# Kernel tuning notes

Hardware: AMD Instinct MI355X
Metric: run time of the kernel (lower is better)

Reference implementation:

```python
import jax, jax.numpy as jnp
import numpy as np

DIM = 512
HEADS = 8
DIM_HEAD = 64
DIM_INNER = HEADS * DIM_HEAD  # 512
EPS = 1e-12


def setup_inputs() -> dict:
    key = jax.random.key(0)
    ks = jax.random.split(key, 5)
    B, X, Y, N = 8, 32, 32, 1024
    fmap = jax.random.normal(ks[0], (B, DIM, X, Y), dtype=jnp.float32)
    context = jax.random.normal(ks[1], (B, N, DIM), dtype=jnp.float32)
    gamma_fmap = jnp.ones((DIM, 1, 1), dtype=jnp.float32)
    gamma_ctx = jnp.ones((DIM,), dtype=jnp.float32)
    Wq = jax.random.normal(ks[2], (DIM_INNER, DIM), dtype=jnp.float32) * 0.02
    Wkv = jax.random.normal(ks[3], (2 * DIM_INNER, DIM), dtype=jnp.float32) * 0.02
    Wout = jax.random.normal(ks[4], (DIM, DIM_INNER), dtype=jnp.float32) * 0.02
    return {"fmap": fmap, "context": context, "gamma_fmap": gamma_fmap,
            "gamma_ctx": gamma_ctx, "Wq": Wq, "Wkv": Wkv, "Wout": Wout}


def _channel_rmsnorm(x, gamma):
    # F.normalize(x, dim=1) * sqrt(dim) * gamma ; x: [b, c, x, y]
    norm = jnp.sqrt(jnp.sum(x * x, axis=1, keepdims=True))
    normed = x / jnp.maximum(norm, EPS)
    return normed * (DIM ** 0.5) * gamma


def _rmsnorm(x, gamma):
    # F.normalize(x, dim=-1) * sqrt(dim) * gamma ; x: [b, n, d]
    norm = jnp.sqrt(jnp.sum(x * x, axis=-1, keepdims=True))
    normed = x / jnp.maximum(norm, EPS)
    return normed * (DIM ** 0.5) * gamma


def reference(fmap, context, gamma_fmap, gamma_ctx, Wq, Wkv, Wout):
    B, _, X, Y = fmap.shape
    N = context.shape[1]
    H, D = HEADS, DIM_HEAD
    scale = D ** -0.5

    fm = _channel_rmsnorm(fmap, gamma_fmap)          # [b, c, x, y]
    ctx = _rmsnorm(context, gamma_ctx)               # [b, n, c]

    # 1x1 conv == channel matmul
    q = jnp.einsum('bcxy,ec->bexy', fm, Wq)          # [b, h*d, x, y]
    kv = jnp.einsum('bnc,ec->bne', ctx, Wkv)         # [b, n, 2*h*d]
    k, v = jnp.split(kv, 2, axis=-1)

    # q: b (h d) x y -> (b h) (x y) d
    q = q.reshape(B, H, D, X * Y).transpose(0, 1, 3, 2).reshape(B * H, X * Y, D)
    # k, v: b n (h d) -> (b h) n d
    k = k.reshape(B, N, H, D).transpose(0, 2, 1, 3).reshape(B * H, N, D)
    v = v.reshape(B, N, H, D).transpose(0, 2, 1, 3).reshape(B * H, N, D)

    # Euclidean cdist: sqrt(||q||^2 + ||k||^2 - 2 q.k)
    q2 = jnp.sum(q * q, axis=-1)                     # [bh, i]
    k2 = jnp.sum(k * k, axis=-1)                     # [bh, j]
    qk = jnp.einsum('bid,bjd->bij', q, k)            # [bh, i, j]
    dist = jnp.sqrt(jnp.maximum(q2[:, :, None] + k2[:, None, :] - 2.0 * qk, 0.0))
    sim = -dist * scale
    attn = jax.nn.softmax(sim, axis=-1)

    out = jnp.einsum('bij,bjd->bid', attn, v)        # [bh, xy, d]
    # (b h) (x y) d -> b (h d) x y
    out = out.reshape(B, H, X * Y, D).transpose(0, 1, 3, 2).reshape(B, H * D, X, Y)
    return jnp.einsum('bexy,de->bdxy', out, Wout)    # [b, dim, x, y]
```

## Files before the change

kernel.cpp:

```cpp
#include <hip/hip_runtime.h>
#include <hip/hip_bf16.h>
#include <math.h>

#define BATCH 8
#define CDIM 512
#define XY 1024
#define NCTX 1024
#define HEADS 8
#define DHEAD 64
#define EINNER 512
#define E2 1024

#define SQRT_DIM 22.627416997969522f
#define NEG_SL2E -0.18033688011112042f

typedef short bf16x8 __attribute__((ext_vector_type(8)));
typedef float f32x4 __attribute__((ext_vector_type(4)));
typedef unsigned short u16;
typedef u16 ushort8v __attribute__((ext_vector_type(8)));
typedef u16 ushort4v __attribute__((ext_vector_type(4)));

__device__ __forceinline__ u16 f2bf(float x) {
    return __builtin_bit_cast(u16, __float2bfloat16(x));
}
__device__ __forceinline__ float bf2f(u16 h) {
    unsigned int u = ((unsigned int)h) << 16;
    return __builtin_bit_cast(float, u);
}

__global__ __launch_bounds__(256) void k_fmap_prep(const float* __restrict__ fmap,
                                                   u16* __restrict__ fmTh,
                                                   u16* __restrict__ fmTl,
                                                   float* __restrict__ fscale) {
    const int blk = blockIdx.x, b = blk >> 5, x0 = (blk & 31) * 32;
    const int xy = threadIdx.x & 31, cg = threadIdx.x >> 5;
    const float* p = fmap + (size_t)b * CDIM * XY + x0 + xy;
    u16* ph = fmTh + ((size_t)b * 1024 + x0 + xy) * 512 + cg * 64;
    u16* pl = fmTl + ((size_t)b * 1024 + x0 + xy) * 512 + cg * 64;
    float ss = 0.f;
#pragma unroll
    for (int ii = 0; ii < 8; ++ii) {
        ushort8v h8, l8;
#pragma unroll
        for (int j = 0; j < 8; ++j) {
            float v = p[(size_t)(cg * 64 + ii * 8 + j) * XY];
            ss = fmaf(v, v, ss);
            u16 hh = f2bf(v);
            h8[j] = hh;
            l8[j] = f2bf(v - bf2f(hh));
        }
        *(ushort8v*)(ph + ii * 8) = h8;
        *(ushort8v*)(pl + ii * 8) = l8;
    }
    __shared__ float red[8][33];
    red[cg][xy] = ss;
    __syncthreads();
    if (threadIdx.x < 32) {
        float s = red[0][xy] + red[1][xy] + red[2][xy] + red[3][xy]
                + red[4][xy] + red[5][xy] + red[6][xy] + red[7][xy];
        fscale[b * XY + x0 + xy] = SQRT_DIM / fmaxf(sqrtf(s), 1e-12f);
    }
}

__global__ __launch_bounds__(256) void k_ctx_scale(const float* __restrict__ ctx,
                                                   float* __restrict__ cscale) {
    int row = blockIdx.x * 4 + (threadIdx.x >> 6);
    int lane = threadIdx.x & 63;
    const float* p = ctx + (size_t)row * CDIM;
    float ss = 0.f;
#pragma unroll
    for (int k = 0; k < CDIM / 64; ++k) {
        float v = p[lane + 64 * k];
        ss = fmaf(v, v, ss);
    }
#pragma unroll
    for (int off = 32; off; off >>= 1) ss += __shfl_down(ss, off, 64);
    if (lane == 0) cscale[row] = SQRT_DIM / fmaxf(sqrtf(ss), 1e-12f);
}

__global__ __launch_bounds__(256) void k_wsplit(const float* __restrict__ src,
                                                const float* __restrict__ gamma,
                                                u16* __restrict__ dh,
                                                u16* __restrict__ dl, int n8) {
    int i = blockIdx.x * 256 + threadIdx.x;
    if (i >= n8) return;
    size_t base = (size_t)i * 8;
    int k0 = (int)(base & 511);
    float4 a = *(const float4*)(src + base);
    float4 b4 = *(const float4*)(src + base + 4);
    float v[8] = {a.x, a.y, a.z, a.w, b4.x, b4.y, b4.z, b4.w};
    if (gamma) {
        float4 g0 = *(const float4*)(gamma + k0);
        float4 g1 = *(const float4*)(gamma + k0 + 4);
        v[0] *= g0.x; v[1] *= g0.y; v[2] *= g0.z; v[3] *= g0.w;
        v[4] *= g1.x; v[5] *= g1.y; v[6] *= g1.z; v[7] *= g1.w;
    }
    ushort8v h8, l8;
#pragma unroll
    for (int j = 0; j < 8; ++j) {
        u16 hh = f2bf(v[j]);
        h8[j] = hh;
        l8[j] = f2bf(v[j] - bf2f(hh));
    }
    *(ushort8v*)(dh + base) = h8;
    *(ushort8v*)(dl + base) = l8;
}

__global__ __launch_bounds__(256, 4) void k_gemm_q(
    const u16* __restrict__ fmTh, const u16* __restrict__ fmTl,
    const u16* __restrict__ wqh, const u16* __restrict__ wql,
    const float* __restrict__ fscale,
    u16* __restrict__ qh_, u16* __restrict__ ql_, float* __restrict__ q2g) {
    const int b = blockIdx.z, h = blockIdx.y, xy0 = blockIdx.x * 64;
    const int t = threadIdx.x, w = t >> 6, lane = t & 63;
    const int c = lane & 15, g = lane >> 4;
    const u16* Ah = fmTh + ((size_t)b * 1024 + xy0 + 16 * w + c) * 512 + 8 * g;
    const u16* Al = fmTl + ((size_t)b * 1024 + xy0 + 16 * w + c) * 512 + 8 * g;
    const u16* Bh0 = wqh + ((size_t)(h * 64) + c) * 512 + 8 * g;
    const u16* Bl0 = wql + ((size_t)(h * 64) + c) * 512 + 8 * g;
    f32x4 acc[4] = {{0.f,0.f,0.f,0.f},{0.f,0.f,0.f,0.f},{0.f,0.f,0.f,0.f},{0.f,0.f,0.f,0.f}};
#pragma unroll 2
    for (int k0 = 0; k0 < 512; k0 += 32) {
        bf16x8 ah = *(const bf16x8*)(Ah + k0);
        bf16x8 al = *(const bf16x8*)(Al + k0);
#pragma unroll
        for (int ct = 0; ct < 4; ++ct) {
            bf16x8 bh_ = *(const bf16x8*)(Bh0 + (size_t)ct * 16 * 512 + k0);
            bf16x8 bl_ = *(const bf16x8*)(Bl0 + (size_t)ct * 16 * 512 + k0);
            acc[ct] = __builtin_amdgcn_mfma_f32_16x16x32_bf16(ah, bh_, acc[ct], 0, 0, 0);
            acc[ct] = __builtin_amdgcn_mfma_f32_16x16x32_bf16(ah, bl_, acc[ct], 0, 0, 0);
            acc[ct] = __builtin_amdgcn_mfma_f32_16x16x32_bf16(al, bh_, acc[ct], 0, 0, 0);
        }
    }
    const int bh = b * 8 + h;
    const float4 fs4 = *(const float4*)(fscale + b * 1024 + xy0 + 16 * w + 4 * g);
    const float fsr[4] = {fs4.x, fs4.y, fs4.z, fs4.w};
    float s2[4] = {0.f, 0.f, 0.f, 0.f};
#pragma unroll
    for (int ct = 0; ct < 4; ++ct)
#pragma unroll
        for (int r = 0; r < 4; ++r) {
            float v = acc[ct][r] * fsr[r];
            u16 hh = f2bf(v);
            size_t adr = ((size_t)bh * 1024 + xy0 + 16 * w + 4 * g + r) * 64 + 16 * ct + c;
            qh_[adr] = hh;
            ql_[adr] = f2bf(v - bf2f(hh));
            s2[r] = fmaf(v, v, s2[r]);
        }
#pragma unroll
    for (int r = 0; r < 4; ++r) {
        float s = s2[r];
        s += __shfl_xor(s, 1, 64);
        s += __shfl_xor(s, 2, 64);
        s += __shfl_xor(s, 4, 64);
        s += __shfl_xor(s, 8, 64);
        if (c == 0) q2g[(size_t)bh * 1024 + xy0 + 16 * w + 4 * g + r] = s;
    }
}

__global__ __launch_bounds__(256, 4) void k_gemm_kv(
    const float* __restrict__ ctx, const u16* __restrict__ wkvh,
    const u16* __restrict__ wkvl, const float* __restrict__ cscale,
    u16* __restrict__ khi, u16* __restrict__ klo,
    u16* __restrict__ vthi, u16* __restrict__ vtlo, float* __restrict__ k2g) {
    const int b = blockIdx.z, et = blockIdx.y, n0 = blockIdx.x * 64;
    const int t = threadIdx.x, w = t >> 6, lane = t & 63;
    const int c = lane & 15, g = lane >> 4;
    __shared__ u16 vl[4][2][64][24];
    const float* Ap = ctx + ((size_t)b * 1024 + n0 + 16 * w + c) * 512 + 8 * g;
    const u16* Bh0 = wkvh + ((size_t)(et * 64) + c) * 512 + 8 * g;
    const u16* Bl0 = wkvl + ((size_t)(et * 64) + c) * 512 + 8 * g;
    f32x4 acc[4] = {{0.f,0.f,0.f,0.f},{0.f,0.f,0.f,0.f},{0.f,0.f,0.f,0.f},{0.f,0.f,0.f,0.f}};
#pragma unroll 2
    for (int k0 = 0; k0 < 512; k0 += 32) {
        float4 a0 = *(const float4*)(Ap + k0);
        float4 a1 = *(const float4*)(Ap + k0 + 4);
        float av[8] = {a0.x, a0.y, a0.z, a0.w, a1.x, a1.y, a1.z, a1.w};
        bf16x8 ah, al;
#pragma unroll
        for (int j = 0; j < 8; ++j) {
            u16 hh = f2bf(av[j]);
            ah[j] = (short)hh;
            al[j] = (short)f2bf(av[j] - bf2f(hh));
        }
#pragma unroll
        for (int ct = 0; ct < 4; ++ct) {
            bf16x8 bh_ = *(const bf16x8*)(Bh0 + (size_t)ct * 16 * 512 + k0);
            bf16x8 bl_ = *(const bf16x8*)(Bl0 + (size_t)ct * 16 * 512 + k0);
            acc[ct] = __builtin_amdgcn_mfma_f32_16x16x32_bf16(ah, bh_, acc[ct], 0, 0, 0);
            acc[ct] = __builtin_amdgcn_mfma_f32_16x16x32_bf16(ah, bl_, acc[ct], 0, 0, 0);
            acc[ct] = __builtin_amdgcn_mfma_f32_16x16x32_bf16(al, bh_, acc[ct], 0, 0, 0);
        }
    }
    const float4 cs4 = *(const float4*)(cscale + b * 1024 + n0 + 16 * w + 4 * g);
    const float csr[4] = {cs4.x, cs4.y, cs4.z, cs4.w};
    if (et < 8) {
        const int bh = b * 8 + et;
        float s2[4] = {0.f, 0.f, 0.f, 0.f};
#pragma unroll
        for (int ct = 0; ct < 4; ++ct)
#pragma unroll
            for (int r = 0; r < 4; ++r) {
                float v = acc[ct][r] * csr[r];
                u16 hh = f2bf(v);
                size_t adr = ((size_t)bh * 1024 + n0 + 16 * w + 4 * g + r) * 64 + 16 * ct + c;
                khi[adr] = hh;
                klo[adr] = f2bf(v - bf2f(hh));
                s2[r] = fmaf(v, v, s2[r]);
            }
#pragma unroll
        for (int r = 0; r < 4; ++r) {
            float s = s2[r];
            s += __shfl_xor(s, 1, 64);
            s += __shfl_xor(s, 2, 64);
            s += __shfl_xor(s, 4, 64);
            s += __shfl_xor(s, 8, 64);
            if (c == 0) k2g[(size_t)bh * 1024 + n0 + 16 * w + 4 * g + r] = s;
        }
    } else {
        const int h = et - 8, bh = b * 8 + h;
#pragma unroll
        for (int ct = 0; ct < 4; ++ct)
#pragma unroll
            for (int r = 0; r < 4; ++r) {
                float v = acc[ct][r] * csr[r];
                u16 hh = f2bf(v);
                vl[w][0][16 * ct + c][4 * g + r] = hh;
                vl[w][1][16 * ct + c][4 * g + r] = f2bf(v - bf2f(hh));
            }
        const int d = lane;
        ushort8v h0 = *(const ushort8v*)(&vl[w][0][d][0]);
        ushort8v h1 = *(const ushort8v*)(&vl[w][0][d][8]);
        ushort8v l0 = *(const ushort8v*)(&vl[w][1][d][0]);
        ushort8v l1 = *(const ushort8v*)(&vl[w][1][d][8]);
        size_t base = ((size_t)bh * 64 + d) * 1024 + n0 + 16 * w;
        *(ushort8v*)(vthi + base) = h0;
        *(ushort8v*)(vthi + base + 8) = h1;
        *(ushort8v*)(vtlo + base) = l0;
        *(ushort8v*)(vtlo + base + 8) = l1;
    }
}

__global__ __launch_bounds__(256, 4) void k_gemm_out(
    const u16* __restrict__ wouth, const u16* __restrict__ woutl,
    const u16* __restrict__ aoTh, const u16* __restrict__ aoTl,
    float* __restrict__ out) {
    const int b = blockIdx.z, m0 = blockIdx.y * 64, n0 = blockIdx.x * 64;
    const int t = threadIdx.x, w = t >> 6, lane = t & 63;
    const int c = lane & 15, g = lane >> 4;
    const u16* Ah = wouth + ((size_t)(m0 + 16 * w) + c) * 512 + 8 * g;
    const u16* Al = woutl + ((size_t)(m0 + 16 * w) + c) * 512 + 8 * g;
    const u16* Bh0 = aoTh + ((size_t)b * 1024 + n0 + c) * 512 + 8 * g;
    const u16* Bl0 = aoTl + ((size_t)b * 1024 + n0 + c) * 512 + 8 * g;
    f32x4 acc[4] = {{0.f,0.f,0.f,0.f},{0.f,0.f,0.f,0.f},{0.f,0.f,0.f,0.f},{0.f,0.f,0.f,0.f}};
#pragma unroll 2
    for (int k0 = 0; k0 < 512; k0 += 32) {
        bf16x8 ah = *(const bf16x8*)(Ah + k0);
        bf16x8 al = *(const bf16x8*)(Al + k0);
#pragma unroll
        for (int ct = 0; ct < 4; ++ct) {
            bf16x8 bh_ = *(const bf16x8*)(Bh0 + (size_t)ct * 16 * 512 + k0);
            bf16x8 bl_ = *(const bf16x8*)(Bl0 + (size_t)ct * 16 * 512 + k0);
            acc[ct] = __builtin_amdgcn_mfma_f32_16x16x32_bf16(ah, bh_, acc[ct], 0, 0, 0);
            acc[ct] = __builtin_amdgcn_mfma_f32_16x16x32_bf16(ah, bl_, acc[ct], 0, 0, 0);
            acc[ct] = __builtin_amdgcn_mfma_f32_16x16x32_bf16(al, bh_, acc[ct], 0, 0, 0);
        }
    }
#pragma unroll
    for (int ct = 0; ct < 4; ++ct)
#pragma unroll
        for (int r = 0; r < 4; ++r)
            out[((size_t)b * 512 + m0 + 16 * w + 4 * g + r) * 1024 + n0 + 16 * ct + c] =
                acc[ct][r];
}

__global__ __launch_bounds__(256, 4) void k_attn_mfma(
    const u16* __restrict__ q_h, const u16* __restrict__ q_l,
    const u16* __restrict__ khi, const u16* __restrict__ klo,
    const u16* __restrict__ vthi, const u16* __restrict__ vtlo,
    const float* __restrict__ q2g, const float* __restrict__ k2g,
    u16* __restrict__ aoTh, u16* __restrict__ aoTl) {
    const int bh = blockIdx.x;
    const int i0 = blockIdx.y * 32;
    const int t = threadIdx.x;
    const int w = t >> 6;
    const int rg = w >> 1;
    const int jh = w & 1;
    const int lane = t & 63;
    const int c = lane & 15, g = lane >> 4;

    __shared__ __align__(16) char pool[4 * 4864];
    u16* psth = (u16*)(pool + w * 4864);
    u16* pstl = psth + 16 * 76;
    __shared__ float msh[4][16];
    __shared__ float lsh[4][16];

    const int qrow = i0 + 16 * rg + c;
    const u16* qhp = q_h + ((size_t)bh * 1024 + qrow) * 64 + 8 * g;
    const u16* qlp = q_l + ((size_t)bh * 1024 + qrow) * 64 + 8 * g;
    bf16x8 qh[2], ql[2];
    qh[0] = *(const bf16x8*)(qhp);
    qh[1] = *(const bf16x8*)(qhp + 32);
    ql[0] = *(const bf16x8*)(qlp);
    ql[1] = *(const bf16x8*)(qlp + 32);
    const float q2c = q2g[(size_t)bh * 1024 + qrow];

    const u16* khb = khi + (size_t)bh * NCTX * 64;
    const u16* klb = klo + (size_t)bh * NCTX * 64;
    const u16* vhb = vthi + (size_t)bh * 64 * NCTX;
    const u16* vlb = vtlo + (size_t)bh * 64 * NCTX;
    const float* k2b = k2g + (size_t)bh * NCTX;

    f32x4 acc_o[4] = {{0.f,0.f,0.f,0.f},{0.f,0.f,0.f,0.f},{0.f,0.f,0.f,0.f},{0.f,0.f,0.f,0.f}};
    float m_run = -1e30f, l_run = 0.f;

    const int jbeg = jh * 512, jend = jbeg + 512;
    for (int j0 = jbeg; j0 < jend; j0 += 64) {
        float s[4][4];
#pragma unroll
        for (int mm = 0; mm < 4; ++mm) {
            const u16* kr_h = khb + (size_t)(j0 + 16 * mm + c) * 64 + 8 * g;
            const u16* kr_l = klb + (size_t)(j0 + 16 * mm + c) * 64 + 8 * g;
            f32x4 acc = {0.f, 0.f, 0.f, 0.f};
#pragma unroll
            for (int kk = 0; kk < 2; ++kk) {
                bf16x8 kh_ = *(const bf16x8*)(kr_h + 32 * kk);
                bf16x8 kl_ = *(const bf16x8*)(kr_l + 32 * kk);
                acc = __builtin_amdgcn_mfma_f32_16x16x32_bf16(kh_, qh[kk], acc, 0, 0, 0);
                acc = __builtin_amdgcn_mfma_f32_16x16x32_bf16(kh_, ql[kk], acc, 0, 0, 0);
                acc = __builtin_amdgcn_mfma_f32_16x16x32_bf16(kl_, qh[kk], acc, 0, 0, 0);
            }
            const float4 kv4 = *(const float4*)(k2b + j0 + 16 * mm + 4 * g);
            const float k2a[4] = {kv4.x, kv4.y, kv4.z, kv4.w};
#pragma unroll
            for (int r = 0; r < 4; ++r) {
                float d2 = fmaf(-2.f, acc[r], q2c + k2a[r]);
                s[mm][r] = NEG_SL2E * sqrtf(fmaxf(d2, 0.f));
            }
        }
        float mt = s[0][0];
#pragma unroll
        for (int mm = 0; mm < 4; ++mm)
#pragma unroll
            for (int r = 0; r < 4; ++r) mt = fmaxf(mt, s[mm][r]);
        mt = fmaxf(mt, __shfl_xor(mt, 16, 64));
        mt = fmaxf(mt, __shfl_xor(mt, 32, 64));
        float mn = fmaxf(m_run, mt);
        float alpha = exp2f(m_run - mn);
        m_run = mn;
        float sum = 0.f;
#pragma unroll
        for (int mm = 0; mm < 4; ++mm)
#pragma unroll
            for (int r = 0; r < 4; ++r) {
                float e = exp2f(s[mm][r] - mn);
                s[mm][r] = e;
                sum += e;
            }
        sum += __shfl_xor(sum, 16, 64);
        sum += __shfl_xor(sum, 32, 64);
        l_run = l_run * alpha + sum;
#pragma unroll
        for (int dt = 0; dt < 4; ++dt)
#pragma unroll
            for (int r = 0; r < 4; ++r) acc_o[dt][r] *= alpha;

#pragma unroll
        for (int mm = 0; mm < 4; ++mm) {
            ushort4v h4, l4;
#pragma unroll
            for (int r = 0; r < 4; ++r) {
                u16 hh = f2bf(s[mm][r]);
                h4[r] = hh;
                l4[r] = f2bf(s[mm][r] - bf2f(hh));
            }
            *(ushort4v*)(psth + c * 76 + 16 * mm + 4 * g) = h4;
            *(ushort4v*)(pstl + c * 76 + 16 * mm + 4 * g) = l4;
        }
        bf16x8 ph[2], pl[2];
#pragma unroll
        for (int kk = 0; kk < 2; ++kk) {
            ph[kk] = *(const bf16x8*)(psth + c * 76 + 32 * kk + 8 * g);
            pl[kk] = *(const bf16x8*)(pstl + c * 76 + 32 * kk + 8 * g);
        }
#pragma unroll
        for (int dt = 0; dt < 4; ++dt) {
            const u16* vr_h = vhb + (size_t)(16 * dt + c) * NCTX + j0 + 8 * g;
            const u16* vr_l = vlb + (size_t)(16 * dt + c) * NCTX + j0 + 8 * g;
#pragma unroll
            for (int kk = 0; kk < 2; ++kk) {
                bf16x8 vh_ = *(const bf16x8*)(vr_h + 32 * kk);
                bf16x8 vl_ = *(const bf16x8*)(vr_l + 32 * kk);
                acc_o[dt] = __builtin_amdgcn_mfma_f32_16x16x32_bf16(vh_, ph[kk], acc_o[dt], 0, 0, 0);
                acc_o[dt] = __builtin_amdgcn_mfma_f32_16x16x32_bf16(vh_, pl[kk], acc_o[dt], 0, 0, 0);
                acc_o[dt] = __builtin_amdgcn_mfma_f32_16x16x32_bf16(vl_, ph[kk], acc_o[dt], 0, 0, 0);
            }
        }
    }

    float* pfw = (float*)(pool + w * 4864);
#pragma unroll
    for (int dt = 0; dt < 4; ++dt)
#pragma unroll
        for (int r = 0; r < 4; ++r)
            pfw[(16 * dt + 4 * g + r) * 18 + c] = acc_o[dt][r];
    if (g == 0) { msh[w][c] = m_run; lsh[w][c] = l_run; }
    __syncthreads();

    {
        const int cq = t & 15, rgq = (t >> 4) & 1, dblk = t >> 5;
        const int wA = 2 * rgq, wB = wA + 1;
        const float m1 = msh[wA][cq], m2 = msh[wB][cq];
        const float l1 = lsh[wA][cq], l2 = lsh[wB][cq];
        const float M = fmaxf(m1, m2);
        const float e1 = exp2f(m1 - M), e2 = exp2f(m2 - M);
        const float inv = 1.f / (e1 * l1 + e2 * l2);
        const float w1 = e1 * inv, w2 = e2 * inv;
        const float* pA = (const float*)(pool + wA * 4864);
        const float* pB = (const float*)(pool + wB * 4864);
        const int b = bh >> 3, h = bh & 7;
        const int xy = i0 + 16 * rgq + cq;
        ushort8v h8, l8;
#pragma unroll
        for (int dd = 0; dd < 8; ++dd) {
            int d = dblk * 8 + dd;
            float o = w1 * pA[d * 18 + cq] + w2 * pB[d * 18 + cq];
            u16 hh = f2bf(o);
            h8[dd] = hh;
            l8[dd] = f2bf(o - bf2f(hh));
        }
        size_t adr = ((size_t)b * 1024 + xy) * 512 + h * 64 + dblk * 8;
        *(ushort8v*)(aoTh + adr) = h8;
        *(ushort8v*)(aoTl + adr) = l8;
    }
}

extern "C" void kernel_launch(void* const* d_in, const int* in_sizes, int n_in,
                              void* d_out, int out_size, void* d_ws, size_t ws_size,
                              hipStream_t stream) {
    const float* fmap    = (const float*)d_in[0];
    const float* context = (const float*)d_in[1];
    const float* gfm     = (const float*)d_in[2];
    const float* gctx    = (const float*)d_in[3];
    const float* Wq      = (const float*)d_in[4];
    const float* Wkv     = (const float*)d_in[5];
    const float* Wout    = (const float*)d_in[6];
    float* out = (float*)d_out;

    char* wsb = (char*)d_ws;
    u16* fmTh = (u16*)(wsb);
    u16* fmTl = (u16*)(wsb + (8u << 20));
    u16* khi  = fmTh;
    u16* klo  = fmTl;
    u16* vthi = (u16*)(wsb + (16u << 20));
    u16* vtlo = (u16*)(wsb + (24u << 20));
    u16* q_h  = (u16*)(wsb + (32u << 20));
    u16* q_l  = (u16*)(wsb + (40u << 20));
    u16* aoTh = (u16*)(wsb + (48u << 20));
    u16* aoTl = (u16*)(wsb + (56u << 20));
    u16* wouth = (u16*)(wsb);
    u16* woutl = (u16*)(wsb + 524288 * 2);

    u16* du = (u16*)d_out;
    u16* wkvh = du;
    u16* wkvl = du + 524288;
    u16* wqh  = du + 1048576;
    u16* wql  = du + 1310720;
    float* df = (float*)((char*)d_out + (4u << 20));
    float* q2g    = df;
    float* k2g    = df + 65536;
    float* fscale = df + 131072;
    float* cscale = df + 139264;

    k_fmap_prep<<<256, 256, 0, stream>>>(fmap, fmTh, fmTl, fscale);
    k_ctx_scale<<<2048, 256, 0, stream>>>(context, cscale);
    k_wsplit<<<128, 256, 0, stream>>>(Wq, gfm, wqh, wql, 512 * 512 / 8);
    k_wsplit<<<256, 256, 0, stream>>>(Wkv, gctx, wkvh, wkvl, 1024 * 512 / 8);

    k_gemm_q<<<dim3(16, 8, BATCH), 256, 0, stream>>>(
        fmTh, fmTl, wqh, wql, fscale, q_h, q_l, q2g);

    k_gemm_kv<<<dim3(16, 16, BATCH), 256, 0, stream>>>(
        context, wkvh, wkvl, cscale, khi, klo, vthi, vtlo, k2g);

    k_attn_mfma<<<dim3(64, 32), 256, 0, stream>>>(
        q_h, q_l, khi, klo, vthi, vtlo, q2g, k2g, aoTh, aoTl);

    k_wsplit<<<128, 256, 0, stream>>>(Wout, nullptr, wouth, woutl, 512 * 512 / 8);

    k_gemm_out<<<dim3(16, 8, BATCH), 256, 0, stream>>>(
        wouth, woutl, aoTh, aoTl, out);
}
```

Baseline: 653.9 us.

## Pad GEMM row strides, pre-split context to bf16, use fast sqrt/exp in attention

```diff
diff --git a/kernel.cpp b/kernel.cpp
--- a/kernel.cpp
+++ b/kernel.cpp
@@ -11,6 +11,9 @@
 #define EINNER 512
 #define E2 1024
 
+#define GSTR 640
+#define VSTR 1152
+
 #define SQRT_DIM 22.627416997969522f
 #define NEG_SL2E -0.18033688011112042f
 
@@ -26,6 +29,16 @@
 __device__ __forceinline__ float bf2f(u16 h) {
     unsigned int u = ((unsigned int)h) << 16;
     return __builtin_bit_cast(float, u);
+}
+__device__ __forceinline__ float fast_sqrt(float x) {
+    float r;
+    asm("v_sqrt_f32 %0, %1" : "=v"(r) : "v"(x));
+    return r;
+}
+__device__ __forceinline__ float fast_exp2(float x) {
+    float r;
+    asm("v_exp_f32 %0, %1" : "=v"(r) : "v"(x));
+    return r;
 }
 
 __global__ __launch_bounds__(256) void k_fmap_prep(const float* __restrict__ fmap,
@@ -35,8 +48,8 @@
     const int blk = blockIdx.x, b = blk >> 5, x0 = (blk & 31) * 32;
     const int xy = threadIdx.x & 31, cg = threadIdx.x >> 5;
     const float* p = fmap + (size_t)b * CDIM * XY + x0 + xy;
-    u16* ph = fmTh + ((size_t)b * 1024 + x0 + xy) * 512 + cg * 64;
-    u16* pl = fmTl + ((size_t)b * 1024 + x0 + xy) * 512 + cg * 64;
+    u16* ph = fmTh + ((size_t)b * 1024 + x0 + xy) * GSTR + cg * 64;
+    u16* pl = fmTl + ((size_t)b * 1024 + x0 + xy) * GSTR + cg * 64;
     float ss = 0.f;
 #pragma unroll
     for (int ii = 0; ii < 8; ++ii) {
@@ -62,17 +75,27 @@
     }
 }
 
-__global__ __launch_bounds__(256) void k_ctx_scale(const float* __restrict__ ctx,
-                                                   float* __restrict__ cscale) {
-    int row = blockIdx.x * 4 + (threadIdx.x >> 6);
-    int lane = threadIdx.x & 63;
-    const float* p = ctx + (size_t)row * CDIM;
+__global__ __launch_bounds__(256) void k_ctx_prep(const float* __restrict__ ctx,
+                                                  u16* __restrict__ ctxh,
+                                                  u16* __restrict__ ctxl,
+                                                  float* __restrict__ cscale) {
+    const int row = blockIdx.x * 4 + (threadIdx.x >> 6);
+    const int lane = threadIdx.x & 63;
+    const float* p = ctx + (size_t)row * CDIM + lane * 8;
+    float4 a0 = *(const float4*)(p);
+    float4 a1 = *(const float4*)(p + 4);
+    float v[8] = {a0.x, a0.y, a0.z, a0.w, a1.x, a1.y, a1.z, a1.w};
     float ss = 0.f;
-#pragma unroll
-    for (int k = 0; k < CDIM / 64; ++k) {
-        float v = p[lane + 64 * k];
-        ss = fmaf(v, v, ss);
-    }
+    ushort8v h8, l8;
+#pragma unroll
+    for (int j = 0; j < 8; ++j) {
+        ss = fmaf(v[j], v[j], ss);
+        u16 hh = f2bf(v[j]);
+        h8[j] = hh;
+        l8[j] = f2bf(v[j] - bf2f(hh));
+    }
+    *(ushort8v*)(ctxh + (size_t)row * GSTR + lane * 8) = h8;
+    *(ushort8v*)(ctxl + (size_t)row * GSTR + lane * 8) = l8;
 #pragma unroll
     for (int off = 32; off; off >>= 1) ss += __shfl_down(ss, off, 64);
     if (lane == 0) cscale[row] = SQRT_DIM / fmaxf(sqrtf(ss), 1e-12f);
@@ -86,6 +109,7 @@
     if (i >= n8) return;
     size_t base = (size_t)i * 8;
     int k0 = (int)(base & 511);
+    size_t row = base >> 9;
     float4 a = *(const float4*)(src + base);
     float4 b4 = *(const float4*)(src + base + 4);
     float v[8] = {a.x, a.y, a.z, a.w, b4.x, b4.y, b4.z, b4.w};
@@ -102,8 +126,9 @@
         h8[j] = hh;
         l8[j] = f2bf(v[j] - bf2f(hh));
     }
-    *(ushort8v*)(dh + base) = h8;
-    *(ushort8v*)(dl + base) = l8;
+    size_t dst = row * GSTR + k0;
+    *(ushort8v*)(dh + dst) = h8;
+    *(ushort8v*)(dl + dst) = l8;
 }
 
 __global__ __launch_bounds__(256, 4) void k_gemm_q(
@@ -114,10 +139,10 @@
     const int b = blockIdx.z, h = blockIdx.y, xy0 = blockIdx.x * 64;
     const int t = threadIdx.x, w = t >> 6, lane = t & 63;
     const int c = lane & 15, g = lane >> 4;
-    const u16* Ah = fmTh + ((size_t)b * 1024 + xy0 + 16 * w + c) * 512 + 8 * g;
-    const u16* Al = fmTl + ((size_t)b * 1024 + xy0 + 16 * w + c) * 512 + 8 * g;
-    const u16* Bh0 = wqh + ((size_t)(h * 64) + c) * 512 + 8 * g;
-    const u16* Bl0 = wql + ((size_t)(h * 64) + c) * 512 + 8 * g;
+    const u16* Ah = fmTh + ((size_t)b * 1024 + xy0 + 16 * w + c) * GSTR + 8 * g;
+    const u16* Al = fmTl + ((size_t)b * 1024 + xy0 + 16 * w + c) * GSTR + 8 * g;
+    const u16* Bh0 = wqh + ((size_t)(h * 64) + c) * GSTR + 8 * g;
+    const u16* Bl0 = wql + ((size_t)(h * 64) + c) * GSTR + 8 * g;
     f32x4 acc[4] = {{0.f,0.f,0.f,0.f},{0.f,0.f,0.f,0.f},{0.f,0.f,0.f,0.f},{0.f,0.f,0.f,0.f}};
 #pragma unroll 2
     for (int k0 = 0; k0 < 512; k0 += 32) {
@@ -125,8 +150,8 @@
         bf16x8 al = *(const bf16x8*)(Al + k0);
 #pragma unroll
         for (int ct = 0; ct < 4; ++ct) {
-            bf16x8 bh_ = *(const bf16x8*)(Bh0 + (size_t)ct * 16 * 512 + k0);
-            bf16x8 bl_ = *(const bf16x8*)(Bl0 + (size_t)ct * 16 * 512 + k0);
+            bf16x8 bh_ = *(const bf16x8*)(Bh0 + (size_t)ct * 16 * GSTR + k0);
+            bf16x8 bl_ = *(const bf16x8*)(Bl0 + (size_t)ct * 16 * GSTR + k0);
             acc[ct] = __builtin_amdgcn_mfma_f32_16x16x32_bf16(ah, bh_, acc[ct], 0, 0, 0);
             acc[ct] = __builtin_amdgcn_mfma_f32_16x16x32_bf16(ah, bl_, acc[ct], 0, 0, 0);
             acc[ct] = __builtin_amdgcn_mfma_f32_16x16x32_bf16(al, bh_, acc[ct], 0, 0, 0);
@@ -159,34 +184,28 @@
 }
 
 __global__ __launch_bounds__(256, 4) void k_gemm_kv(
-    const float* __restrict__ ctx, const u16* __restrict__ wkvh,
-    const u16* __restrict__ wkvl, const float* __restrict__ cscale,
+    const u16* __restrict__ ctxh, const u16* __restrict__ ctxl,
+    const u16* __restrict__ wkvh, const u16* __restrict__ wkvl,
+    const float* __restrict__ cscale,
     u16* __restrict__ khi, u16* __restrict__ klo,
     u16* __restrict__ vthi, u16* __restrict__ vtlo, float* __restrict__ k2g) {
     const int b = blockIdx.z, et = blockIdx.y, n0 = blockIdx.x * 64;
     const int t = threadIdx.x, w = t >> 6, lane = t & 63;
     const int c = lane & 15, g = lane >> 4;
     __shared__ u16 vl[4][2][64][24];
-    const float* Ap = ctx + ((size_t)b * 1024 + n0 + 16 * w + c) * 512 + 8 * g;
-    const u16* Bh0 = wkvh + ((size_t)(et * 64) + c) * 512 + 8 * g;
-    const u16* Bl0 = wkvl + ((size_t)(et * 64) + c) * 512 + 8 * g;
+    const u16* Ah = ctxh + ((size_t)b * 1024 + n0 + 16 * w + c) * GSTR + 8 * g;
+    const u16* Al = ctxl + ((size_t)b * 1024 + n0 + 16 * w + c) * GSTR + 8 * g;
+    const u16* Bh0 = wkvh + ((size_t)(et * 64) + c) * GSTR + 8 * g;
+    const u16* Bl0 = wkvl + ((size_t)(et * 64) + c) * GSTR + 8 * g;
     f32x4 acc[4] = {{0.f,0.f,0.f,0.f},{0.f,0.f,0.f,0.f},{0.f,0.f,0.f,0.f},{0.f,0.f,0.f,0.f}};
 #pragma unroll 2
     for (int k0 = 0; k0 < 512; k0 += 32) {
-        float4 a0 = *(const float4*)(Ap + k0);
-        float4 a1 = *(const float4*)(Ap + k0 + 4);
-        float av[8] = {a0.x, a0.y, a0.z, a0.w, a1.x, a1.y, a1.z, a1.w};
-        bf16x8 ah, al;
-#pragma unroll
-        for (int j = 0; j < 8; ++j) {
-            u16 hh = f2bf(av[j]);
-            ah[j] = (short)hh;
-            al[j] = (short)f2bf(av[j] - bf2f(hh));
-        }
+        bf16x8 ah = *(const bf16x8*)(Ah + k0);
+        bf16x8 al = *(const bf16x8*)(Al + k0);
 #pragma unroll
         for (int ct = 0; ct < 4; ++ct) {
-            bf16x8 bh_ = *(const bf16x8*)(Bh0 + (size_t)ct * 16 * 512 + k0);
-            bf16x8 bl_ = *(const bf16x8*)(Bl0 + (size_t)ct * 16 * 512 + k0);
+            bf16x8 bh_ = *(const bf16x8*)(Bh0 + (size_t)ct * 16 * GSTR + k0);
+            bf16x8 bl_ = *(const bf16x8*)(Bl0 + (size_t)ct * 16 * GSTR + k0);
             acc[ct] = __builtin_amdgcn_mfma_f32_16x16x32_bf16(ah, bh_, acc[ct], 0, 0, 0);
             acc[ct] = __builtin_amdgcn_mfma_f32_16x16x32_bf16(ah, bl_, acc[ct], 0, 0, 0);
             acc[ct] = __builtin_amdgcn_mfma_f32_16x16x32_bf16(al, bh_, acc[ct], 0, 0, 0);
@@ -233,7 +252,7 @@
         ushort8v h1 = *(const ushort8v*)(&vl[w][0][d][8]);
         ushort8v l0 = *(const ushort8v*)(&vl[w][1][d][0]);
         ushort8v l1 = *(const ushort8v*)(&vl[w][1][d][8]);
-        size_t base = ((size_t)bh * 64 + d) * 1024 + n0 + 16 * w;
+        size_t base = ((size_t)bh * 64 + d) * VSTR + n0 + 16 * w;
         *(ushort8v*)(vthi + base) = h0;
         *(ushort8v*)(vthi + base + 8) = h1;
         *(ushort8v*)(vtlo + base) = l0;
@@ -248,10 +267,10 @@
     const int b = blockIdx.z, m0 = blockIdx.y * 64, n0 = blockIdx.x * 64;
     const int t = threadIdx.x, w = t >> 6, lane = t & 63;
     const int c = lane & 15, g = lane >> 4;
-    const u16* Ah = wouth + ((size_t)(m0 + 16 * w) + c) * 512 + 8 * g;
-    const u16* Al = woutl + ((size_t)(m0 + 16 * w) + c) * 512 + 8 * g;
-    const u16* Bh0 = aoTh + ((size_t)b * 1024 + n0 + c) * 512 + 8 * g;
-    const u16* Bl0 = aoTl + ((size_t)b * 1024 + n0 + c) * 512 + 8 * g;
+    const u16* Ah = wouth + ((size_t)(m0 + 16 * w) + c) * GSTR + 8 * g;
+    const u16* Al = woutl + ((size_t)(m0 + 16 * w) + c) * GSTR + 8 * g;
+    const u16* Bh0 = aoTh + ((size_t)b * 1024 + n0 + c) * GSTR + 8 * g;
+    const u16* Bl0 = aoTl + ((size_t)b * 1024 + n0 + c) * GSTR + 8 * g;
     f32x4 acc[4] = {{0.f,0.f,0.f,0.f},{0.f,0.f,0.f,0.f},{0.f,0.f,0.f,0.f},{0.f,0.f,0.f,0.f}};
 #pragma unroll 2
     for (int k0 = 0; k0 < 512; k0 += 32) {
@@ -259,8 +278,8 @@
         bf16x8 al = *(const bf16x8*)(Al + k0);
 #pragma unroll
         for (int ct = 0; ct < 4; ++ct) {
-            bf16x8 bh_ = *(const bf16x8*)(Bh0 + (size_t)ct * 16 * 512 + k0);
-            bf16x8 bl_ = *(const bf16x8*)(Bl0 + (size_t)ct * 16 * 512 + k0);
+            bf16x8 bh_ = *(const bf16x8*)(Bh0 + (size_t)ct * 16 * GSTR + k0);
+            bf16x8 bl_ = *(const bf16x8*)(Bl0 + (size_t)ct * 16 * GSTR + k0);
             acc[ct] = __builtin_amdgcn_mfma_f32_16x16x32_bf16(ah, bh_, acc[ct], 0, 0, 0);
             acc[ct] = __builtin_amdgcn_mfma_f32_16x16x32_bf16(ah, bl_, acc[ct], 0, 0, 0);
             acc[ct] = __builtin_amdgcn_mfma_f32_16x16x32_bf16(al, bh_, acc[ct], 0, 0, 0);
@@ -305,22 +324,29 @@
     ql[1] = *(const bf16x8*)(qlp + 32);
     const float q2c = q2g[(size_t)bh * 1024 + qrow];
 
-    const u16* khb = khi + (size_t)bh * NCTX * 64;
-    const u16* klb = klo + (size_t)bh * NCTX * 64;
-    const u16* vhb = vthi + (size_t)bh * 64 * NCTX;
-    const u16* vlb = vtlo + (size_t)bh * 64 * NCTX;
-    const float* k2b = k2g + (size_t)bh * NCTX;
+    const int jbeg = jh * 512;
+    const u16* kh_p = khi + (size_t)bh * NCTX * 64 + (size_t)(jbeg + c) * 64 + 8 * g;
+    const u16* kl_p = klo + (size_t)bh * NCTX * 64 + (size_t)(jbeg + c) * 64 + 8 * g;
+    const u16* kh_p2 = kh_p + 2048;
+    const u16* kl_p2 = kl_p + 2048;
+    const float* k2p = k2g + (size_t)bh * NCTX + jbeg + 4 * g;
+    const u16* vh_p[4];
+    const u16* vl_p[4];
+#pragma unroll
+    for (int dt = 0; dt < 4; ++dt) {
+        vh_p[dt] = vthi + ((size_t)bh * 64 + 16 * dt + c) * VSTR + jbeg + 8 * g;
+        vl_p[dt] = vtlo + ((size_t)bh * 64 + 16 * dt + c) * VSTR + jbeg + 8 * g;
+    }
 
     f32x4 acc_o[4] = {{0.f,0.f,0.f,0.f},{0.f,0.f,0.f,0.f},{0.f,0.f,0.f,0.f},{0.f,0.f,0.f,0.f}};
     float m_run = -1e30f, l_run = 0.f;
 
-    const int jbeg = jh * 512, jend = jbeg + 512;
-    for (int j0 = jbeg; j0 < jend; j0 += 64) {
+    for (int it = 0; it < 8; ++it) {
         float s[4][4];
 #pragma unroll
         for (int mm = 0; mm < 4; ++mm) {
-            const u16* kr_h = khb + (size_t)(j0 + 16 * mm + c) * 64 + 8 * g;
-            const u16* kr_l = klb + (size_t)(j0 + 16 * mm + c) * 64 + 8 * g;
+            const u16* kr_h = (mm < 2 ? kh_p : kh_p2) + (mm & 1) * 1024;
+            const u16* kr_l = (mm < 2 ? kl_p : kl_p2) + (mm & 1) * 1024;
             f32x4 acc = {0.f, 0.f, 0.f, 0.f};
 #pragma unroll
             for (int kk = 0; kk < 2; ++kk) {
@@ -330,12 +356,12 @@
                 acc = __builtin_amdgcn_mfma_f32_16x16x32_bf16(kh_, ql[kk], acc, 0, 0, 0);
                 acc = __builtin_amdgcn_mfma_f32_16x16x32_bf16(kl_, qh[kk], acc, 0, 0, 0);
             }
-            const float4 kv4 = *(const float4*)(k2b + j0 + 16 * mm + 4 * g);
+            const float4 kv4 = *(const float4*)(k2p + 16 * mm);
             const float k2a[4] = {kv4.x, kv4.y, kv4.z, kv4.w};
 #pragma unroll
             for (int r = 0; r < 4; ++r) {
                 float d2 = fmaf(-2.f, acc[r], q2c + k2a[r]);
-                s[mm][r] = NEG_SL2E * sqrtf(fmaxf(d2, 0.f));
+                s[mm][r] = NEG_SL2E * fast_sqrt(fmaxf(d2, 0.f));
             }
         }
         float mt = s[0][0];
@@ -346,14 +372,14 @@
         mt = fmaxf(mt, __shfl_xor(mt, 16, 64));
         mt = fmaxf(mt, __shfl_xor(mt, 32, 64));
         float mn = fmaxf(m_run, mt);
-        float alpha = exp2f(m_run - mn);
+        float alpha = fast_exp2(m_run - mn);
         m_run = mn;
         float sum = 0.f;
 #pragma unroll
         for (int mm = 0; mm < 4; ++mm)
 #pragma unroll
             for (int r = 0; r < 4; ++r) {
-                float e = exp2f(s[mm][r] - mn);
+                float e = fast_exp2(s[mm][r] - mn);
                 s[mm][r] = e;
                 sum += e;
             }
@@ -385,17 +411,19 @@
         }
 #pragma unroll
         for (int dt = 0; dt < 4; ++dt) {
-            const u16* vr_h = vhb + (size_t)(16 * dt + c) * NCTX + j0 + 8 * g;
-            const u16* vr_l = vlb + (size_t)(16 * dt + c) * NCTX + j0 + 8 * g;
 #pragma unroll
             for (int kk = 0; kk < 2; ++kk) {
-                bf16x8 vh_ = *(const bf16x8*)(vr_h + 32 * kk);
-                bf16x8 vl_ = *(const bf16x8*)(vr_l + 32 * kk);
+                bf16x8 vh_ = *(const bf16x8*)(vh_p[dt] + 32 * kk);
+                bf16x8 vl_ = *(const bf16x8*)(vl_p[dt] + 32 * kk);
                 acc_o[dt] = __builtin_amdgcn_mfma_f32_16x16x32_bf16(vh_, ph[kk], acc_o[dt], 0, 0, 0);
                 acc_o[dt] = __builtin_amdgcn_mfma_f32_16x16x32_bf16(vh_, pl[kk], acc_o[dt], 0, 0, 0);
                 acc_o[dt] = __builtin_amdgcn_mfma_f32_16x16x32_bf16(vl_, ph[kk], acc_o[dt], 0, 0, 0);
             }
         }
+        kh_p += 4096; kl_p += 4096; kh_p2 += 4096; kl_p2 += 4096;
+        k2p += 64;
+#pragma unroll
+        for (int dt = 0; dt < 4; ++dt) { vh_p[dt] += 64; vl_p[dt] += 64; }
     }
 
     float* pfw = (float*)(pool + w * 4864);
@@ -413,7 +441,7 @@
         const float m1 = msh[wA][cq], m2 = msh[wB][cq];
         const float l1 = lsh[wA][cq], l2 = lsh[wB][cq];
         const float M = fmaxf(m1, m2);
-        const float e1 = exp2f(m1 - M), e2 = exp2f(m2 - M);
+        const float e1 = fast_exp2(m1 - M), e2 = fast_exp2(m2 - M);
         const float inv = 1.f / (e1 * l1 + e2 * l2);
         const float w1 = e1 * inv, w2 = e2 * inv;
         const float* pA = (const float*)(pool + wA * 4864);
@@ -429,7 +457,7 @@
             h8[dd] = hh;
             l8[dd] = f2bf(o - bf2f(hh));
         }
-        size_t adr = ((size_t)b * 1024 + xy) * 512 + h * 64 + dblk * 8;
+        size_t adr = ((size_t)b * 1024 + xy) * GSTR + h * 64 + dblk * 8;
         *(ushort8v*)(aoTh + adr) = h8;
         *(ushort8v*)(aoTl + adr) = l8;
     }
@@ -449,31 +477,32 @@
 
     char* wsb = (char*)d_ws;
     u16* fmTh = (u16*)(wsb);
-    u16* fmTl = (u16*)(wsb + (8u << 20));
+    u16* fmTl = (u16*)(wsb + (10u << 20));
     u16* khi  = fmTh;
     u16* klo  = fmTl;
-    u16* vthi = (u16*)(wsb + (16u << 20));
-    u16* vtlo = (u16*)(wsb + (24u << 20));
-    u16* q_h  = (u16*)(wsb + (32u << 20));
-    u16* q_l  = (u16*)(wsb + (40u << 20));
-    u16* aoTh = (u16*)(wsb + (48u << 20));
-    u16* aoTl = (u16*)(wsb + (56u << 20));
-    u16* wouth = (u16*)(wsb);
-    u16* woutl = (u16*)(wsb + 524288 * 2);
-
-    u16* du = (u16*)d_out;
-    u16* wkvh = du;
-    u16* wkvl = du + 524288;
-    u16* wqh  = du + 1048576;
-    u16* wql  = du + 1310720;
-    float* df = (float*)((char*)d_out + (4u << 20));
-    float* q2g    = df;
-    float* k2g    = df + 65536;
-    float* fscale = df + 131072;
-    float* cscale = df + 139264;
+    u16* wouth = fmTh;
+    u16* woutl = (u16*)(wsb + (1u << 20));
+    u16* vthi = (u16*)(wsb + (20u << 20));
+    u16* vtlo = (u16*)(wsb + (29u << 20));
+    u16* ctxh = (u16*)(wsb + (38u << 20));
+    u16* ctxl = (u16*)(wsb + (48u << 20));
+    u16* aoTh = ctxh;
+    u16* aoTl = ctxl;
+    char* r6 = wsb + (58u << 20);
+    u16* wqh  = (u16*)(r6);
+    u16* wql  = (u16*)(r6 + 655360);
+    u16* wkvh = (u16*)(r6 + 1310720);
+    u16* wkvl = (u16*)(r6 + 2621440);
+    float* q2g    = (float*)(r6 + 3932160);
+    float* k2g    = q2g + 65536;
+    float* fscale = k2g + 65536;
+    float* cscale = fscale + 8192;
+
+    u16* q_h = (u16*)d_out;
+    u16* q_l = q_h + 4194304;
 
     k_fmap_prep<<<256, 256, 0, stream>>>(fmap, fmTh, fmTl, fscale);
-    k_ctx_scale<<<2048, 256, 0, stream>>>(context, cscale);
+    k_ctx_prep<<<2048, 256, 0, stream>>>(context, ctxh, ctxl, cscale);
     k_wsplit<<<128, 256, 0, stream>>>(Wq, gfm, wqh, wql, 512 * 512 / 8);
     k_wsplit<<<256, 256, 0, stream>>>(Wkv, gctx, wkvh, wkvl, 1024 * 512 / 8);
 
@@ -481,7 +510,7 @@
         fmTh, fmTl, wqh, wql, fscale, q_h, q_l, q2g);
 
     k_gemm_kv<<<dim3(16, 16, BATCH), 256, 0, stream>>>(
-        context, wkvh, wkvl, cscale, khi, klo, vthi, vtlo, k2g);
+        ctxh, ctxl, wkvh, wkvl, cscale, khi, klo, vthi, vtlo, k2g);
 
     k_attn_mfma<<<dim3(64, 32), 256, 0, stream>>>(
         q_h, q_l, khi, klo, vthi, vtlo, q2g, k2g, aoTh, aoTl);
```

Result: no change. 653.3 us (-0.1%).
